# Optimization experiments

Measured on AMD Instinct MI355X. Metric: run time of the kernel, lower is better.

## Reference

```python
import jax, jax.numpy as jnp
import numpy as np

# Fixed by module source: forward hardcodes a 200x200 BEV grid, dim=128,
# MSDeformAttn(n_levels=1, n_heads=4, n_points=8).
B, Z, X, C, H, P = 2, 200, 200, 128, 4, 8
N = Z * X
D = C // H  # head dim = 32


def setup_inputs() -> dict:
    key = jax.random.key(0)
    ks = jax.random.split(key, 12)
    s = 0.02
    return {
        "query": jax.random.normal(ks[0], (B, N, C), jnp.float32),
        # MSDeformAttn.value_proj
        "Wv": jax.random.normal(ks[1], (C, C), jnp.float32) * s,
        "bv": jnp.zeros((C,), jnp.float32),
        # MSDeformAttn.sampling_offsets (C -> H*1*P*2)
        "Woff": jax.random.normal(ks[2], (C, H * P * 2), jnp.float32) * s,
        "boff": jax.random.normal(ks[3], (H * P * 2,), jnp.float32) * 2.0,
        # MSDeformAttn.attention_weights (C -> H*1*P)
        "Wattn": jax.random.normal(ks[4], (C, H * P), jnp.float32) * s,
        "battn": jnp.zeros((H * P,), jnp.float32),
        # MSDeformAttn.output_proj
        "Wout1": jax.random.normal(ks[5], (C, C), jnp.float32) * s,
        "bout1": jnp.zeros((C,), jnp.float32),
        # VanillaSelfAttention.output_proj
        "Wout2": jax.random.normal(ks[6], (C, C), jnp.float32) * s,
        "bout2": jnp.zeros((C,), jnp.float32),
    }


def _forward(query, Wv, bv, Woff, boff, Wattn, battn, Wout1, bout1, Wout2, bout2):
    # Reference points: normalized centers of the 200x200 grid, order (z, x).
    zc = (jnp.arange(Z, dtype=jnp.float32) + 0.5) / Z
    xc = (jnp.arange(X, dtype=jnp.float32) + 0.5) / X
    ref = jnp.stack(jnp.meshgrid(zc, xc, indexing="ij"), axis=-1).reshape(N, 2)

    # value_proj on input_flatten (== query); split heads, lay out as images.
    value = (query @ Wv + bv).reshape(B, Z, X, H, D)
    value_flat = value.transpose(0, 3, 1, 2, 4).reshape(B * H, Z * X, D)  # (BH, ZX, D)

    # Sampling locations: ref + offsets / offset_normalizer ([W, H] = [200, 200]).
    off = (query @ Woff + boff).reshape(B, N, H, P, 2)
    norm = jnp.array([X, Z], jnp.float32)
    loc = ref[None, :, None, None, :] + off / norm  # (B, N, H, P, 2)

    # Attention weights: softmax over n_levels*n_points (= P here).
    attn = jax.nn.softmax((query @ Wattn + battn).reshape(B, N, H, P), axis=-1)

    # grid_sample convention: grid = 2*loc - 1, grid[...,0]=x (width), align_corners=False.
    grid = 2.0 * loc - 1.0
    ix = ((grid[..., 0] + 1.0) * X - 1.0) * 0.5  # pixel x coords
    iy = ((grid[..., 1] + 1.0) * Z - 1.0) * 0.5  # pixel y coords
    ix = ix.transpose(0, 2, 1, 3).reshape(B * H, N * P)
    iy = iy.transpose(0, 2, 1, 3).reshape(B * H, N * P)

    x0f = jnp.floor(ix); y0f = jnp.floor(iy)
    lx = ix - x0f; ly = iy - y0f
    x0 = x0f.astype(jnp.int32); y0 = y0f.astype(jnp.int32)
    x1 = x0 + 1; y1 = y0 + 1

    def corner(xi, yi, w):
        # zero padding: out-of-bounds corners contribute 0
        valid = (xi >= 0) & (xi < X) & (yi >= 0) & (yi < Z)
        idx = jnp.clip(yi, 0, Z - 1) * X + jnp.clip(xi, 0, X - 1)  # (BH, N*P)
        v = jnp.take_along_axis(value_flat, idx[..., None], axis=1)  # (BH, N*P, D)
        return v * (w * valid.astype(w.dtype))[..., None]

    sampled = (
        corner(x0, y0, (1.0 - lx) * (1.0 - ly))
        + corner(x1, y0, lx * (1.0 - ly))
        + corner(x0, y1, (1.0 - lx) * ly)
        + corner(x1, y1, lx * ly)
    ).reshape(B, H, N, P, D)

    # Weighted reduce over points, merge heads.
    out = jnp.einsum("bhnpd,bnhp->bnhd", sampled, attn).reshape(B, N, C)
    out = out @ Wout1 + bout1  # MSDeformAttn.output_proj
    out = out @ Wout2 + bout2  # VanillaSelfAttention.output_proj
    return out + query  # dropout is identity in eval; residual add


def reference(query, Wv, bv, Woff, boff, Wattn, battn, Wout1, bout1, Wout2, bout2):
    return _forward(query, Wv, bv, Woff, boff, Wattn, battn, Wout1, bout1, Wout2, bout2)
```

## Files before the change

### kernel.cpp

```cpp
#include <hip/hip_runtime.h>
#include <hip/hip_bf16.h>
#include <cstddef>

namespace {
constexpr int B  = 2;
constexpr int Z  = 200;
constexpr int X  = 200;
constexpr int C  = 128;
constexpr int H  = 4;
constexpr int P  = 8;
constexpr int N  = Z * X;
constexpr int BN = B * N;
constexpr int SC = 96;
constexpr int NF_P = 14;
constexpr int NF_O = 8;
constexpr int KS   = 4;

typedef __attribute__((ext_vector_type(8))) short short8;
typedef __attribute__((ext_vector_type(4))) float f32x4;
typedef __attribute__((ext_vector_type(2))) float f32x2;
typedef _Float16 h16x2 __attribute__((ext_vector_type(2)));

__device__ inline ushort f2bf(float x) {
    __hip_bfloat16 h = __float2bfloat16(x);
    return *reinterpret_cast<ushort*>(&h);
}
__device__ inline unsigned packbf(float a, float b) {
    return (unsigned)f2bf(a) | ((unsigned)f2bf(b) << 16);
}
__device__ inline ushort f2h(float x) {
    _Float16 h = (_Float16)x;
    return __builtin_bit_cast(ushort, h);
}
__device__ inline float h1f(ushort u) {
    return (float)__builtin_bit_cast(_Float16, u);
}
__device__ inline float2 h2f2(unsigned u) {
    h16x2 h = __builtin_bit_cast(h16x2, u);
    return make_float2((float)h[0], (float)h[1]);
}
template <int MASK>
__device__ inline float swzx(float x) {
    constexpr int pat = (MASK << 10) | 0x1F;
    return __int_as_float(__builtin_amdgcn_ds_swizzle(__float_as_int(x), pat));
}
}

__global__ __launch_bounds__(256) void vsa_k_prep(
    const float* __restrict__ Wv,    const float* __restrict__ bv,
    const float* __restrict__ Woff,  const float* __restrict__ boff,
    const float* __restrict__ Wattn, const float* __restrict__ battn,
    const float* __restrict__ Wout1, const float* __restrict__ bout1,
    const float* __restrict__ Wout2, const float* __restrict__ bout2,
    ushort* __restrict__ wtp, ushort* __restrict__ wtp2,
    float* __restrict__ biasp, float* __restrict__ bias2)
{
    const int u = blockIdx.x * 256 + threadIdx.x;
    constexpr int NP = KS * NF_P * 64;
    constexpr int NO = KS * NF_O * 64;

    if (u < NP) {
        int ks  = u / (NF_P * 64);
        int rem = u - ks * (NF_P * 64);
        int f = rem >> 6, l = rem & 63;
        int n  = f * 16 + (l & 15);
        int kb = ks * 32 + (l >> 4) * 8;
        float v[8];
        #pragma unroll
        for (int e = 0; e < 8; ++e) {
            int k = kb + e;
            if (n < 128)      v[e] = Wv[k * 128 + n];
            else if (n < 192) v[e] = Woff[k * 64 + (n - 128)];
            else              v[e] = Wattn[k * 32 + (n - 192)];
        }
        unsigned* dst = (unsigned*)(wtp + (size_t)u * 8);
        #pragma unroll
        for (int i = 0; i < 4; ++i) dst[i] = packbf(v[2*i], v[2*i+1]);
    } else if (u < NP + NO) {
        int t   = u - NP;
        int ks  = t / (NF_O * 64);
        int rem = t - ks * (NF_O * 64);
        int f = rem >> 6, l = rem & 63;
        int n  = f * 16 + (l & 15);
        int kb = ks * 32 + (l >> 4) * 8;
        float acc[8] = {0,0,0,0,0,0,0,0};
        for (int j = 0; j < 128; ++j) {
            float w2 = Wout2[j * 128 + n];
            #pragma unroll
            for (int e = 0; e < 8; ++e)
                acc[e] = fmaf(Wout1[(kb + e) * 128 + j], w2, acc[e]);
        }
        unsigned* dst = (unsigned*)(wtp2 + (size_t)t * 8);
        #pragma unroll
        for (int i = 0; i < 4; ++i) dst[i] = packbf(acc[2*i], acc[2*i+1]);
    } else if (u < NP + NO + 224) {
        int c = u - NP - NO;
        float bb;
        if (c < 128)      bb = bv[c];
        else if (c < 192) bb = boff[c - 128];
        else              bb = battn[c - 192];
        biasp[c] = bb;
    } else if (u < NP + NO + 224 + 128) {
        int c = u - NP - NO - 224;
        float acc = bout2[c];
        for (int j = 0; j < 128; ++j)
            acc = fmaf(bout1[j], Wout2[j * 128 + c], acc);
        bias2[c] = acc;
    }
}

__global__ __launch_bounds__(256) void vsa_k_proj(
    const float* __restrict__ Q, const ushort* __restrict__ wtp,
    const float* __restrict__ biasp,
    unsigned char* __restrict__ proj_v8, ushort* __restrict__ proj_s16)
{
    const int lane = threadIdx.x & 63;
    const int wave = blockIdx.x * 4 + (threadIdx.x >> 6);
    const int row0 = wave * 16;
    const int m  = lane & 15;
    const int kg = lane >> 4;

    const float* qp = Q + (size_t)(row0 + m) * 128 + kg * 8;

    f32x4 acc[NF_P];
    #pragma unroll
    for (int f = 0; f < NF_P; ++f) acc[f] = (f32x4){0.f, 0.f, 0.f, 0.f};

    #pragma unroll
    for (int ks = 0; ks < KS; ++ks) {
        float4 a0 = *(const float4*)(qp + ks * 32);
        float4 a1 = *(const float4*)(qp + ks * 32 + 4);
        short8 af;
        af[0] = (short)f2bf(a0.x); af[1] = (short)f2bf(a0.y);
        af[2] = (short)f2bf(a0.z); af[3] = (short)f2bf(a0.w);
        af[4] = (short)f2bf(a1.x); af[5] = (short)f2bf(a1.y);
        af[6] = (short)f2bf(a1.z); af[7] = (short)f2bf(a1.w);
        const short8* wrow = (const short8*)wtp + ks * NF_P * 64 + lane;
        #pragma unroll
        for (int f = 0; f < NF_P; ++f)
            acc[f] = __builtin_amdgcn_mfma_f32_16x16x32_bf16(af, wrow[f * 64], acc[f], 0, 0, 0);
    }

    #pragma unroll
    for (int f = 0; f < 8; ++f) {
        const int col = f * 16 + m;
        const float bb = biasp[col];
        #pragma unroll
        for (int r = 0; r < 4; ++r) {
            const float v = acc[f][r] + bb;
            const int pk = __builtin_amdgcn_cvt_pk_fp8_f32(v, v, 0, false);
            proj_v8[(size_t)(row0 + kg * 4 + r) * 128 + col] = (unsigned char)pk;
        }
    }
    #pragma unroll
    for (int f = 8; f < 12; ++f) {
        const int col = f * 16 + m;
        const float bb = biasp[col];
        #pragma unroll
        for (int r = 0; r < 4; ++r)
            proj_s16[(size_t)(row0 + kg * 4 + r) * SC + (col - 128)] = f2h(acc[f][r] + bb);
    }
    #pragma unroll
    for (int f = 12; f < 14; ++f) {
        const float bb = biasp[f * 16 + m];
        #pragma unroll
        for (int r = 0; r < 4; ++r) {
            float v = acc[f][r] + bb;
            float mx = v;
            mx = fmaxf(mx, swzx<1>(mx));
            mx = fmaxf(mx, swzx<2>(mx));
            mx = fmaxf(mx, swzx<4>(mx));
            float ex = __expf(v - mx);
            float sm = ex;
            sm += swzx<1>(sm); sm += swzx<2>(sm); sm += swzx<4>(sm);
            const float wp = ex / sm;
            proj_s16[(size_t)(row0 + kg * 4 + r) * SC + 64 + (f - 12) * 16 + m] = f2h(wp);
        }
    }
}

__global__ __launch_bounds__(256) void vsa_k_sample(
    const unsigned char* __restrict__ proj_v8, const ushort* __restrict__ proj_s16,
    ushort* __restrict__ tmp)
{
    const int lane  = threadIdx.x & 63;
    const int w     = threadIdx.x >> 6;
    const int pixb  = w >> 1;
    const int hpair = w & 1;
    const int h     = hpair * 2 + (lane >> 5);
    const int p     = (lane >> 2) & 7;
    const int d8    = lane & 3;

    const int orig = blockIdx.x;
    const int wg   = (orig & 7) * 5000 + (orig >> 3);
    const int b    = wg / 20000;
    const int r2   = wg - b * 20000;
    const int j    = r2 / 100;
    const int i    = (r2 - j * 100) * 2 + pixb;
    const int bn   = b * N + i * X + j;

    const ushort* srow = proj_s16 + (size_t)bn * SC;
    const unsigned char* vb = proj_v8 + (size_t)b * N * 128;

    const float2 off = h2f2(*(const unsigned*)(srow + (h * 8 + p) * 2));
    const float  wp  = h1f(srow[64 + h * 8 + p]);

    const float ixf = (float)i + off.x;
    const float iyf = (float)j + off.y;
    const float x0f = floorf(ixf), y0f = floorf(iyf);
    const float lx = ixf - x0f, ly = iyf - y0f;
    const int x0 = (int)x0f, y0 = (int)y0f;
    const int x1 = x0 + 1,  y1 = y0 + 1;
    const int xc0 = min(max(x0, 0), X - 1), xc1 = min(max(x1, 0), X - 1);
    const int yc0 = min(max(y0, 0), Z - 1), yc1 = min(max(y1, 0), Z - 1);

    const float wx0 = ((unsigned)x0 < (unsigned)X) ? (1.f - lx) : 0.f;
    const float wx1 = ((unsigned)x1 < (unsigned)X) ? lx : 0.f;
    const float wy0 = (((unsigned)y0 < (unsigned)Z) ? (1.f - ly) : 0.f) * wp;
    const float wy1 = (((unsigned)y1 < (unsigned)Z) ? ly : 0.f) * wp;
    const float w00 = wx0 * wy0, w10 = wx1 * wy0;
    const float w01 = wx0 * wy1, w11 = wx1 * wy1;

    const int rb0 = yc0 * X, rb1 = yc1 * X;
    const int hb  = h * 32 + d8 * 8;

    const uint2 c00 = *(const uint2*)(vb + (rb0 + xc0) * 128 + hb);
    const uint2 c10 = *(const uint2*)(vb + (rb0 + xc1) * 128 + hb);
    const uint2 c01 = *(const uint2*)(vb + (rb1 + xc0) * 128 + hb);
    const uint2 c11 = *(const uint2*)(vb + (rb1 + xc1) * 128 + hb);

    float a0 = 0.f, a1 = 0.f, a2 = 0.f, a3 = 0.f;
    float a4 = 0.f, a5 = 0.f, a6 = 0.f, a7 = 0.f;
    #define VSA_ACC(c, wgt) { \
        f32x2 u0 = __builtin_amdgcn_cvt_pk_f32_fp8((int)(c).x, false); \
        f32x2 u1 = __builtin_amdgcn_cvt_pk_f32_fp8((int)(c).x, true);  \
        f32x2 u2 = __builtin_amdgcn_cvt_pk_f32_fp8((int)(c).y, false); \
        f32x2 u3 = __builtin_amdgcn_cvt_pk_f32_fp8((int)(c).y, true);  \
        a0 = fmaf(wgt, u0.x, a0); a1 = fmaf(wgt, u0.y, a1); \
        a2 = fmaf(wgt, u1.x, a2); a3 = fmaf(wgt, u1.y, a3); \
        a4 = fmaf(wgt, u2.x, a4); a5 = fmaf(wgt, u2.y, a5); \
        a6 = fmaf(wgt, u3.x, a6); a7 = fmaf(wgt, u3.y, a7); }
    VSA_ACC(c00, w00)
    VSA_ACC(c10, w10)
    VSA_ACC(c01, w01)
    VSA_ACC(c11, w11)
    #undef VSA_ACC

    a0 += swzx<4>(a0);  a1 += swzx<4>(a1);  a2 += swzx<4>(a2);  a3 += swzx<4>(a3);
    a4 += swzx<4>(a4);  a5 += swzx<4>(a5);  a6 += swzx<4>(a6);  a7 += swzx<4>(a7);
    a0 += swzx<8>(a0);  a1 += swzx<8>(a1);  a2 += swzx<8>(a2);  a3 += swzx<8>(a3);
    a4 += swzx<8>(a4);  a5 += swzx<8>(a5);  a6 += swzx<8>(a6);  a7 += swzx<8>(a7);
    a0 += swzx<16>(a0); a1 += swzx<16>(a1); a2 += swzx<16>(a2); a3 += swzx<16>(a3);
    a4 += swzx<16>(a4); a5 += swzx<16>(a5); a6 += swzx<16>(a6); a7 += swzx<16>(a7);

    if (p == 0) {
        uint4 o;
        o.x = packbf(a0, a1);
        o.y = packbf(a2, a3);
        o.z = packbf(a4, a5);
        o.w = packbf(a6, a7);
        *(uint4*)(tmp + (size_t)bn * 128 + h * 32 + d8 * 8) = o;
    }
}

__global__ __launch_bounds__(256) void vsa_k_out(
    const ushort* __restrict__ tmp, const ushort* __restrict__ wtp2,
    const float* __restrict__ bias2, const float* __restrict__ Q,
    float* __restrict__ out)
{
    const int lane = threadIdx.x & 63;
    const int wave = blockIdx.x * 4 + (threadIdx.x >> 6);
    const int row0 = wave * 16;
    const int m  = lane & 15;
    const int kg = lane >> 4;

    const ushort* ap = tmp + (size_t)(row0 + m) * 128 + kg * 8;

    f32x4 acc[NF_O];
    #pragma unroll
    for (int f = 0; f < NF_O; ++f) acc[f] = (f32x4){0.f, 0.f, 0.f, 0.f};

    #pragma unroll
    for (int ks = 0; ks < KS; ++ks) {
        short8 af = *(const short8*)(ap + ks * 32);
        const short8* wrow = (const short8*)wtp2 + ks * NF_O * 64 + lane;
        #pragma unroll
        for (int f = 0; f < NF_O; ++f)
            acc[f] = __builtin_amdgcn_mfma_f32_16x16x32_bf16(af, wrow[f * 64], acc[f], 0, 0, 0);
    }

    #pragma unroll
    for (int f = 0; f < NF_O; ++f) {
        const int col = f * 16 + m;
        const float bb = bias2[col];
        #pragma unroll
        for (int r = 0; r < 4; ++r) {
            const int row = row0 + kg * 4 + r;
            out[(size_t)row * 128 + col] = acc[f][r] + bb + Q[(size_t)row * 128 + col];
        }
    }
}

extern "C" void kernel_launch(void* const* d_in, const int* in_sizes, int n_in,
                              void* d_out, int out_size, void* d_ws, size_t ws_size,
                              hipStream_t stream) {
    const float* Q     = (const float*)d_in[0];
    const float* Wv    = (const float*)d_in[1];
    const float* bv    = (const float*)d_in[2];
    const float* Woff  = (const float*)d_in[3];
    const float* boff  = (const float*)d_in[4];
    const float* Wattn = (const float*)d_in[5];
    const float* battn = (const float*)d_in[6];
    const float* Wout1 = (const float*)d_in[7];
    const float* bout1 = (const float*)d_in[8];
    const float* Wout2 = (const float*)d_in[9];
    const float* bout2 = (const float*)d_in[10];
    float* out = (float*)d_out;

    float*  biasp  = (float*)d_ws;
    float*  bias2  = biasp + 224;
    ushort* proj_s16 = (ushort*)(bias2 + 128);
    unsigned char* proj_v8 = (unsigned char*)(proj_s16 + (size_t)BN * SC);
    ushort* tmp    = (ushort*)(proj_v8 + (size_t)BN * 128);
    ushort* wtp    = tmp + (size_t)BN * 128;
    ushort* wtp2   = wtp + (size_t)KS * NF_P * 64 * 8;

    constexpr int prep_n = KS * NF_P * 64 + KS * NF_O * 64 + 224 + 128;
    vsa_k_prep<<<(prep_n + 255) / 256, 256, 0, stream>>>(
        Wv, bv, Woff, boff, Wattn, battn, Wout1, bout1, Wout2, bout2,
        wtp, wtp2, biasp, bias2);
    vsa_k_proj<<<BN / 64, 256, 0, stream>>>(Q, wtp, biasp, proj_v8, proj_s16);
    vsa_k_sample<<<dim3((Z / 2) * X * B), 256, 0, stream>>>(proj_v8, proj_s16, tmp);
    vsa_k_out<<<BN / 64, 256, 0, stream>>>(tmp, wtp2, bias2, Q, out);
}
```

Measured before the change: 98.54 us.

## Switch value storage to fp16 with packed half FMA sampling and interleaved offsets

Value projections are now stored as fp16 instead of fp8. The sampling kernel accumulates bilinear corners with packed half2 FMAs and does its cross-lane reductions in fp16, which removes the fp8 unpacking and halves the number of FMAs and swizzles. The offset and weight layout is interleaved so each point is fetched with a single 8-byte load. The intermediate buffer and output weights move to fp16 with an f16 MFMA. In exchange the value gathers move twice as many bytes, and accumulating in fp16 carries some rounding risk.

```diff
diff --git a/kernel.cpp b/kernel.cpp
--- a/kernel.cpp
+++ b/kernel.cpp
@@ -11,14 +11,13 @@
 constexpr int P  = 8;
 constexpr int N  = Z * X;
 constexpr int BN = B * N;
-constexpr int SC = 96;
+constexpr int SC = 128;
 constexpr int NF_P = 14;
 constexpr int NF_O = 8;
 constexpr int KS   = 4;
 
 typedef __attribute__((ext_vector_type(8))) short short8;
 typedef __attribute__((ext_vector_type(4))) float f32x4;
-typedef __attribute__((ext_vector_type(2))) float f32x2;
 typedef _Float16 h16x2 __attribute__((ext_vector_type(2)));
 
 __device__ inline ushort f2bf(float x) {
@@ -38,11 +37,23 @@
 __device__ inline float2 h2f2(unsigned u) {
     h16x2 h = __builtin_bit_cast(h16x2, u);
     return make_float2((float)h[0], (float)h[1]);
+}
+__device__ inline unsigned packh(float a, float b) {
+    return (unsigned)f2h(a) | ((unsigned)f2h(b) << 16);
+}
+__device__ inline h16x2 pkrtz(float a, float b) {
+    return __builtin_bit_cast(h16x2, __builtin_amdgcn_cvt_pkrtz(a, b));
 }
 template <int MASK>
 __device__ inline float swzx(float x) {
     constexpr int pat = (MASK << 10) | 0x1F;
     return __int_as_float(__builtin_amdgcn_ds_swizzle(__float_as_int(x), pat));
+}
+template <int MASK>
+__device__ inline h16x2 swzh(h16x2 x) {
+    constexpr int pat = (MASK << 10) | 0x1F;
+    int t = __builtin_amdgcn_ds_swizzle(__builtin_bit_cast(int, x), pat);
+    return __builtin_bit_cast(h16x2, t);
 }
 }
 
@@ -92,7 +103,7 @@
         }
         unsigned* dst = (unsigned*)(wtp2 + (size_t)t * 8);
         #pragma unroll
-        for (int i = 0; i < 4; ++i) dst[i] = packbf(acc[2*i], acc[2*i+1]);
+        for (int i = 0; i < 4; ++i) dst[i] = packh(acc[2*i], acc[2*i+1]);
     } else if (u < NP + NO + 224) {
         int c = u - NP - NO;
         float bb;
@@ -112,7 +123,7 @@
 __global__ __launch_bounds__(256) void vsa_k_proj(
     const float* __restrict__ Q, const ushort* __restrict__ wtp,
     const float* __restrict__ biasp,
-    unsigned char* __restrict__ proj_v8, ushort* __restrict__ proj_s16)
+    ushort* __restrict__ proj_v16, ushort* __restrict__ proj_s16)
 {
     const int lane = threadIdx.x & 63;
     const int wave = blockIdx.x * 4 + (threadIdx.x >> 6);
@@ -146,23 +157,23 @@
         const int col = f * 16 + m;
         const float bb = biasp[col];
         #pragma unroll
-        for (int r = 0; r < 4; ++r) {
-            const float v = acc[f][r] + bb;
-            const int pk = __builtin_amdgcn_cvt_pk_fp8_f32(v, v, 0, false);
-            proj_v8[(size_t)(row0 + kg * 4 + r) * 128 + col] = (unsigned char)pk;
-        }
+        for (int r = 0; r < 4; ++r)
+            proj_v16[(size_t)(row0 + kg * 4 + r) * 128 + col] = f2h(acc[f][r] + bb);
     }
     #pragma unroll
     for (int f = 8; f < 12; ++f) {
         const int col = f * 16 + m;
         const float bb = biasp[col];
+        const int c  = col - 128;
+        const int hp = c >> 1, comp = c & 1;
         #pragma unroll
         for (int r = 0; r < 4; ++r)
-            proj_s16[(size_t)(row0 + kg * 4 + r) * SC + (col - 128)] = f2h(acc[f][r] + bb);
+            proj_s16[(size_t)(row0 + kg * 4 + r) * SC + hp * 4 + comp] = f2h(acc[f][r] + bb);
     }
     #pragma unroll
     for (int f = 12; f < 14; ++f) {
         const float bb = biasp[f * 16 + m];
+        const int hp = (f - 12) * 16 + m;
         #pragma unroll
         for (int r = 0; r < 4; ++r) {
             float v = acc[f][r] + bb;
@@ -174,13 +185,13 @@
             float sm = ex;
             sm += swzx<1>(sm); sm += swzx<2>(sm); sm += swzx<4>(sm);
             const float wp = ex / sm;
-            proj_s16[(size_t)(row0 + kg * 4 + r) * SC + 64 + (f - 12) * 16 + m] = f2h(wp);
+            proj_s16[(size_t)(row0 + kg * 4 + r) * SC + hp * 4 + 2] = f2h(wp);
         }
     }
 }
 
 __global__ __launch_bounds__(256) void vsa_k_sample(
-    const unsigned char* __restrict__ proj_v8, const ushort* __restrict__ proj_s16,
+    const ushort* __restrict__ proj_v16, const ushort* __restrict__ proj_s16,
     ushort* __restrict__ tmp)
 {
     const int lane  = threadIdx.x & 63;
@@ -199,11 +210,9 @@
     const int i    = (r2 - j * 100) * 2 + pixb;
     const int bn   = b * N + i * X + j;
 
-    const ushort* srow = proj_s16 + (size_t)bn * SC;
-    const unsigned char* vb = proj_v8 + (size_t)b * N * 128;
-
-    const float2 off = h2f2(*(const unsigned*)(srow + (h * 8 + p) * 2));
-    const float  wp  = h1f(srow[64 + h * 8 + p]);
+    const uint2 ow = *(const uint2*)(proj_s16 + (size_t)bn * SC + (h * 8 + p) * 4);
+    const float2 off = h2f2(ow.x);
+    const float  wp  = h1f((ushort)(ow.y & 0xffff));
 
     const float ixf = (float)i + off.x;
     const float iyf = (float)j + off.y;
@@ -218,47 +227,43 @@
     const float wx1 = ((unsigned)x1 < (unsigned)X) ? lx : 0.f;
     const float wy0 = (((unsigned)y0 < (unsigned)Z) ? (1.f - ly) : 0.f) * wp;
     const float wy1 = (((unsigned)y1 < (unsigned)Z) ? ly : 0.f) * wp;
-    const float w00 = wx0 * wy0, w10 = wx1 * wy0;
-    const float w01 = wx0 * wy1, w11 = wx1 * wy1;
-
+
+    const h16x2 w00p = pkrtz(wx0 * wy0, wx0 * wy0);
+    const h16x2 w10p = pkrtz(wx1 * wy0, wx1 * wy0);
+    const h16x2 w01p = pkrtz(wx0 * wy1, wx0 * wy1);
+    const h16x2 w11p = pkrtz(wx1 * wy1, wx1 * wy1);
+
+    const ushort* vb = proj_v16 + (size_t)b * N * 128;
     const int rb0 = yc0 * X, rb1 = yc1 * X;
     const int hb  = h * 32 + d8 * 8;
 
-    const uint2 c00 = *(const uint2*)(vb + (rb0 + xc0) * 128 + hb);
-    const uint2 c10 = *(const uint2*)(vb + (rb0 + xc1) * 128 + hb);
-    const uint2 c01 = *(const uint2*)(vb + (rb1 + xc0) * 128 + hb);
-    const uint2 c11 = *(const uint2*)(vb + (rb1 + xc1) * 128 + hb);
-
-    float a0 = 0.f, a1 = 0.f, a2 = 0.f, a3 = 0.f;
-    float a4 = 0.f, a5 = 0.f, a6 = 0.f, a7 = 0.f;
-    #define VSA_ACC(c, wgt) { \
-        f32x2 u0 = __builtin_amdgcn_cvt_pk_f32_fp8((int)(c).x, false); \
-        f32x2 u1 = __builtin_amdgcn_cvt_pk_f32_fp8((int)(c).x, true);  \
-        f32x2 u2 = __builtin_amdgcn_cvt_pk_f32_fp8((int)(c).y, false); \
-        f32x2 u3 = __builtin_amdgcn_cvt_pk_f32_fp8((int)(c).y, true);  \
-        a0 = fmaf(wgt, u0.x, a0); a1 = fmaf(wgt, u0.y, a1); \
-        a2 = fmaf(wgt, u1.x, a2); a3 = fmaf(wgt, u1.y, a3); \
-        a4 = fmaf(wgt, u2.x, a4); a5 = fmaf(wgt, u2.y, a5); \
-        a6 = fmaf(wgt, u3.x, a6); a7 = fmaf(wgt, u3.y, a7); }
-    VSA_ACC(c00, w00)
-    VSA_ACC(c10, w10)
-    VSA_ACC(c01, w01)
-    VSA_ACC(c11, w11)
+    const uint4 c00 = *(const uint4*)(vb + (size_t)(rb0 + xc0) * 128 + hb);
+    const uint4 c10 = *(const uint4*)(vb + (size_t)(rb0 + xc1) * 128 + hb);
+    const uint4 c01 = *(const uint4*)(vb + (size_t)(rb1 + xc0) * 128 + hb);
+    const uint4 c11 = *(const uint4*)(vb + (size_t)(rb1 + xc1) * 128 + hb);
+
+    h16x2 a0 = (h16x2)0, a1 = (h16x2)0, a2 = (h16x2)0, a3 = (h16x2)0;
+    #define VSA_ACC(c, wpk) { \
+        a0 = __builtin_elementwise_fma(__builtin_bit_cast(h16x2, (c).x), wpk, a0); \
+        a1 = __builtin_elementwise_fma(__builtin_bit_cast(h16x2, (c).y), wpk, a1); \
+        a2 = __builtin_elementwise_fma(__builtin_bit_cast(h16x2, (c).z), wpk, a2); \
+        a3 = __builtin_elementwise_fma(__builtin_bit_cast(h16x2, (c).w), wpk, a3); }
+    VSA_ACC(c00, w00p)
+    VSA_ACC(c10, w10p)
+    VSA_ACC(c01, w01p)
+    VSA_ACC(c11, w11p)
     #undef VSA_ACC
 
-    a0 += swzx<4>(a0);  a1 += swzx<4>(a1);  a2 += swzx<4>(a2);  a3 += swzx<4>(a3);
-    a4 += swzx<4>(a4);  a5 += swzx<4>(a5);  a6 += swzx<4>(a6);  a7 += swzx<4>(a7);
-    a0 += swzx<8>(a0);  a1 += swzx<8>(a1);  a2 += swzx<8>(a2);  a3 += swzx<8>(a3);
-    a4 += swzx<8>(a4);  a5 += swzx<8>(a5);  a6 += swzx<8>(a6);  a7 += swzx<8>(a7);
-    a0 += swzx<16>(a0); a1 += swzx<16>(a1); a2 += swzx<16>(a2); a3 += swzx<16>(a3);
-    a4 += swzx<16>(a4); a5 += swzx<16>(a5); a6 += swzx<16>(a6); a7 += swzx<16>(a7);
+    a0 += swzh<4>(a0);  a1 += swzh<4>(a1);  a2 += swzh<4>(a2);  a3 += swzh<4>(a3);
+    a0 += swzh<8>(a0);  a1 += swzh<8>(a1);  a2 += swzh<8>(a2);  a3 += swzh<8>(a3);
+    a0 += swzh<16>(a0); a1 += swzh<16>(a1); a2 += swzh<16>(a2); a3 += swzh<16>(a3);
 
     if (p == 0) {
         uint4 o;
-        o.x = packbf(a0, a1);
-        o.y = packbf(a2, a3);
-        o.z = packbf(a4, a5);
-        o.w = packbf(a6, a7);
+        o.x = __builtin_bit_cast(unsigned, a0);
+        o.y = __builtin_bit_cast(unsigned, a1);
+        o.z = __builtin_bit_cast(unsigned, a2);
+        o.w = __builtin_bit_cast(unsigned, a3);
         *(uint4*)(tmp + (size_t)bn * 128 + h * 32 + d8 * 8) = o;
     }
 }
@@ -286,7 +291,7 @@
         const short8* wrow = (const short8*)wtp2 + ks * NF_O * 64 + lane;
         #pragma unroll
         for (int f = 0; f < NF_O; ++f)
-            acc[f] = __builtin_amdgcn_mfma_f32_16x16x32_bf16(af, wrow[f * 64], acc[f], 0, 0, 0);
+            acc[f] = __builtin_amdgcn_mfma_f32_16x16x32_f16(af, wrow[f * 64], acc[f], 0, 0, 0);
     }
 
     #pragma unroll
@@ -320,8 +325,8 @@
     float*  biasp  = (float*)d_ws;
     float*  bias2  = biasp + 224;
     ushort* proj_s16 = (ushort*)(bias2 + 128);
-    unsigned char* proj_v8 = (unsigned char*)(proj_s16 + (size_t)BN * SC);
-    ushort* tmp    = (ushort*)(proj_v8 + (size_t)BN * 128);
+    ushort* proj_v16 = proj_s16 + (size_t)BN * SC;
+    ushort* tmp    = proj_v16 + (size_t)BN * 128;
     ushort* wtp    = tmp + (size_t)BN * 128;
     ushort* wtp2   = wtp + (size_t)KS * NF_P * 64 * 8;
 
@@ -329,7 +334,7 @@
     vsa_k_prep<<<(prep_n + 255) / 256, 256, 0, stream>>>(
         Wv, bv, Woff, boff, Wattn, battn, Wout1, bout1, Wout2, bout2,
         wtp, wtp2, biasp, bias2);
-    vsa_k_proj<<<BN / 64, 256, 0, stream>>>(Q, wtp, biasp, proj_v8, proj_s16);
-    vsa_k_sample<<<dim3((Z / 2) * X * B), 256, 0, stream>>>(proj_v8, proj_s16, tmp);
+    vsa_k_proj<<<BN / 64, 256, 0, stream>>>(Q, wtp, biasp, proj_v16, proj_s16);
+    vsa_k_sample<<<dim3((Z / 2) * X * B), 256, 0, stream>>>(proj_v16, proj_s16, tmp);
     vsa_k_out<<<BN / 64, 256, 0, stream>>>(tmp, wtp2, bias2, Q, out);
 }
```

Result: faster. 94.81 us (-3.8%).
